# Performance work log

Measured on AMD Instinct MI355X. Metric: run time of the kernel, lower is better.

Reference implementation:

```python
import jax, jax.numpy as jnp
import numpy as np
import math

B, S, D, H = 4, 2048, 1024, 16
HD = D // H  # head_dim = 64


def _rope_tables(max_len, half_dim, theta=10000.0):
    inv_freq = 1.0 / (theta ** (jnp.arange(0, half_dim, dtype=jnp.float32) / half_dim))
    ang = jnp.arange(max_len, dtype=jnp.float32)[:, None] * inv_freq[None, :]  # [max_len, half_dim]
    return jnp.cos(ang), jnp.sin(ang)


def _apply_rope(x, cos, sin):
    # x: [B, H, S, HD]; cos/sin: [S, HD/2]
    x1, x2 = x[..., ::2], x[..., 1::2]
    # matches torch.cat([x1*cos - x2*sin, x1*sin + x2*cos], dim=-1)
    return jnp.concatenate([x1 * cos - x2 * sin, x1 * sin + x2 * cos], axis=-1)


def setup_inputs() -> dict:
    key = jax.random.key(0)
    kx, kq, ko = jax.random.split(key, 3)
    x = jax.random.normal(kx, (B, S, D), dtype=jnp.float32)
    Wqkv = jax.random.normal(kq, (D, 3 * D), dtype=jnp.float32) / math.sqrt(D)
    Wout = jax.random.normal(ko, (D, D), dtype=jnp.float32) / math.sqrt(D)
    cos, sin = _rope_tables(S, HD // 2)
    # causal additive mask, per-batch as in module signature [B, S, S]
    causal = jnp.where(jnp.tril(jnp.ones((S, S), dtype=bool)), 0.0, -1e9).astype(jnp.float32)
    mask = jnp.broadcast_to(causal, (B, S, S))
    return {"x": x, "cos": cos, "sin": sin, "mask": mask, "Wqkv": Wqkv, "Wout": Wout}


def reference(x, cos, sin, mask, Wqkv, Wout):
    b, s, d = x.shape
    qkv = x @ Wqkv  # [B, S, 3D]
    q, k, v = jnp.split(qkv, 3, axis=-1)
    def to_heads(t):
        return t.reshape(b, s, H, HD).transpose(0, 2, 1, 3)  # [B, H, S, HD]
    q, k, v = to_heads(q), to_heads(k), to_heads(v)
    q = _apply_rope(q, cos[:s], sin[:s])
    k = _apply_rope(k, cos[:s], sin[:s])
    scores = jnp.einsum("bhqd,bhkd->bhqk", q, k) / math.sqrt(HD)
    attn = jax.nn.softmax(scores + mask[:, None, :, :], axis=-1)
    out = jnp.einsum("bhqk,bhkd->bhqd", attn, v)  # [B, H, S, HD]
    out = out.transpose(0, 2, 1, 3).reshape(b, s, d)
    return out @ Wout
```

## Files before the change

### kernel.cpp

```cpp
#include <hip/hip_runtime.h>
#include <hip/hip_bf16.h>
#include <stdint.h>

#define B_   4
#define S_   2048
#define D_   1024
#define H_   16
#define HD_  64
#define BH_  (B_*H_)
#define MROWS (B_*S_)

typedef short  short8  __attribute__((ext_vector_type(8)));
typedef float  floatx4 __attribute__((ext_vector_type(4)));

__device__ __forceinline__ ushort f2bf(float f) {
    union { float f; uint32_t u; } v; v.f = f;
    uint32_t u = v.u;
    return (ushort)((u + 0x7FFFu + ((u >> 16) & 1u)) >> 16);
}
__device__ __forceinline__ float u2f(uint32_t u) {
    union { uint32_t u; float f; } v; v.u = u; return v.f;
}
__device__ __forceinline__ uint32_t f2u(float f) {
    union { float f; uint32_t u; } v; v.f = f; return v.u;
}

__device__ __forceinline__ void gl_lds16(const ushort* g, ushort* l) {
    __builtin_amdgcn_global_load_lds(
        (const __attribute__((address_space(1))) unsigned int*)g,
        (__attribute__((address_space(3))) unsigned int*)l,
        16, 0, 0);
}

__global__ void k_f32_to_bf16(const float* __restrict__ in, ushort* __restrict__ out, int n) {
    int i = (blockIdx.x * blockDim.x + threadIdx.x) * 4;
    if (i + 3 < n) {
        float4 f = *(const float4*)(in + i);
        ushort4 o; o.x = f2bf(f.x); o.y = f2bf(f.y); o.z = f2bf(f.z); o.w = f2bf(f.w);
        *(ushort4*)(out + i) = o;
    }
}

__global__ void k_transpose_to_bf16(const float* __restrict__ in, ushort* __restrict__ out,
                                    int R, int C) {
    __shared__ float tile[32][33];
    int bx = blockIdx.x * 32;
    int by = blockIdx.y * 32;
    int tx = threadIdx.x;
    int ty = threadIdx.y;
    #pragma unroll
    for (int j = 0; j < 32; j += 8)
        tile[ty + j][tx] = in[(size_t)(by + ty + j) * C + bx + tx];
    __syncthreads();
    #pragma unroll
    for (int j = 0; j < 32; j += 8)
        out[(size_t)(bx + ty + j) * R + by + tx] = f2bf(tile[tx][ty + j]);
}

__global__ void k_vtrans(const ushort* __restrict__ Vb, ushort* __restrict__ VbT) {
    __shared__ __align__(16) ushort t[64 * 72];
    int bh = blockIdx.x >> 5;
    int s0 = (blockIdx.x & 31) * 64;
    int tid = threadIdx.x;
    int ss = tid >> 2, c0 = (tid & 3) * 16;
    size_t base = (size_t)bh * S_ * HD_;
    *(uint4*)&t[ss * 72 + c0]     = *(const uint4*)&Vb[base + (size_t)(s0 + ss) * HD_ + c0];
    *(uint4*)&t[ss * 72 + c0 + 8] = *(const uint4*)&Vb[base + (size_t)(s0 + ss) * HD_ + c0 + 8];
    __syncthreads();
    int hd = tid >> 2, q0 = (tid & 3) * 16;
    ushort tmp[16];
    #pragma unroll
    for (int e = 0; e < 16; e++) tmp[e] = t[(q0 + e) * 72 + hd];
    size_t obase = (size_t)bh * HD_ * S_ + (size_t)hd * S_ + s0 + q0;
    *(uint4*)&VbT[obase]     = *(const uint4*)&tmp[0];
    *(uint4*)&VbT[obase + 8] = *(const uint4*)&tmp[8];
}

#define BM 128
#define BN 128
#define BK 32
#define LDT 32

template<int EPI>
__global__ __launch_bounds__(256)
void k_gemm(const ushort* __restrict__ A, const ushort* __restrict__ Bt,
            float* __restrict__ outF,
            ushort* __restrict__ q_out, ushort* __restrict__ k_out, ushort* __restrict__ v_out,
            int M, int N, int K) {
    __shared__ __align__(16) ushort As[BM * LDT];
    __shared__ __align__(16) ushort Bs[BN * LDT];
    int tid  = threadIdx.x;
    int lane = tid & 63;
    int wave = tid >> 6;
    int quad = lane >> 4;
    int l16  = lane & 15;
    int bm = blockIdx.y * BM;
    int bn = blockIdx.x * BN;
    int wm = (wave >> 1) * 64;
    int wn = (wave & 1) * 64;

    floatx4 acc[4][4] = {};

    for (int k0 = 0; k0 < K; k0 += BK) {
        __syncthreads();
        #pragma unroll
        for (int p = 0; p < 2; p++) {
            int c   = p * 256 + tid;
            int row = c >> 2;
            int kc  = (c & 3) << 3;
            gl_lds16(&A[(size_t)(bm + row) * K + k0 + kc],  &As[c * 8]);
            gl_lds16(&Bt[(size_t)(bn + row) * K + k0 + kc], &Bs[c * 8]);
        }
        __syncthreads();
        short8 af[4], bf[4];
        #pragma unroll
        for (int mt = 0; mt < 4; mt++)
            af[mt] = *(const short8*)&As[(wm + mt * 16 + l16) * LDT + quad * 8];
        #pragma unroll
        for (int nt = 0; nt < 4; nt++)
            bf[nt] = *(const short8*)&Bs[(wn + nt * 16 + l16) * LDT + quad * 8];
        #pragma unroll
        for (int mt = 0; mt < 4; mt++)
            #pragma unroll
            for (int nt = 0; nt < 4; nt++)
                acc[mt][nt] = __builtin_amdgcn_mfma_f32_16x16x32_bf16(af[mt], bf[nt], acc[mt][nt], 0, 0, 0);
    }

    #pragma unroll
    for (int mt = 0; mt < 4; mt++)
        #pragma unroll
        for (int nt = 0; nt < 4; nt++)
            #pragma unroll
            for (int r = 0; r < 4; r++) {
                int row = bm + wm + mt * 16 + quad * 4 + r;
                int col = bn + wn + nt * 16 + l16;
                float v = acc[mt][nt][r];
                if (EPI == 0) {
                    int which = col >> 10;
                    int rem   = col & 1023;
                    int h  = rem >> 6, hd = rem & 63;
                    int b  = row >> 11, s  = row & 2047;
                    size_t idx = ((size_t)(b * H_ + h) * S_ + s) * HD_ + hd;
                    ushort bv = f2bf(v);
                    ushort* dst = (which == 0) ? q_out : (which == 1) ? k_out : v_out;
                    dst[idx] = bv;
                } else {
                    outF[(size_t)row * N + col] = v;
                }
            }
}

__global__ void k_rope(ushort* __restrict__ Q, ushort* __restrict__ Kv,
                       const float* __restrict__ cosT, const float* __restrict__ sinT) {
    int wid  = (blockIdx.x * 256 + threadIdx.x) >> 6;
    int lane = threadIdx.x & 63;
    int s  = wid & (S_ - 1);
    int bh = wid >> 11;
    int i  = lane & 31;
    float c  = cosT[s * 32 + i];
    float sn = sinT[s * 32 + i];
    size_t base = ((size_t)bh * S_ + s) * HD_;

    uint32_t uq = *(const uint32_t*)&Q[base + 2 * i];
    float x1 = u2f(uq << 16), x2 = u2f(uq & 0xFFFF0000u);
    float o  = (lane < 32) ? (x1 * c - x2 * sn) : (x1 * sn + x2 * c);
    Q[base + lane] = f2bf(o * 0.1803368801f);

    uint32_t uk = *(const uint32_t*)&Kv[base + 2 * i];
    x1 = u2f(uk << 16); x2 = u2f(uk & 0xFFFF0000u);
    o  = (lane < 32) ? (x1 * c - x2 * sn) : (x1 * sn + x2 * c);
    Kv[base + lane] = f2bf(o);
}

__global__ __launch_bounds__(256, 4)
void k_attn(const ushort* __restrict__ Q, const ushort* __restrict__ K,
            const ushort* __restrict__ VT, ushort* __restrict__ O) {
    __shared__ __align__(16) ushort Ksp[2][64 * 32];
    __shared__ __align__(16) ushort Vtp[2][64 * 32];
    __shared__ __align__(16) ushort Pst[4][32 * 72];

    int tid  = threadIdx.x;
    int lane = tid & 63;
    int wave = tid >> 6;
    int quad = lane >> 4;
    int l16  = lane & 15;

    int bh   = blockIdx.x & 63;
    int qblk = 15 - (blockIdx.x >> 6);
    int qb0  = qblk * 128;
    size_t hbase = (size_t)bh * S_ * HD_;
    size_t vbase = (size_t)bh * HD_ * S_;

    int mrow[2] = { qb0 + wave * 16, qb0 + 64 + wave * 16 };

    short8 qf[2][2];
    #pragma unroll
    for (int m = 0; m < 2; m++)
        #pragma unroll
        for (int h = 0; h < 2; h++)
            qf[m][h] = *(const short8*)&Q[hbase + (size_t)(mrow[m] + l16) * HD_ + quad * 8 + h * 32];

    short8 ones;
    #pragma unroll
    for (int e = 0; e < 8; e++) ones[e] = (short)0x3F80;

    floatx4 acc[2][4] = {};
    floatx4 accl[2] = {};

    int crow = tid >> 2;
    int coff = (tid & 3) * 8;

    int nk = 2 * qblk + 2;
    for (int kb = 0; kb < nk; kb++) {
        int k0 = kb * 64;
        __syncthreads();
        #pragma unroll
        for (int h = 0; h < 2; h++)
            gl_lds16(&K[hbase + (size_t)(k0 + crow) * HD_ + h * 32 + coff], &Ksp[h][tid * 8]);
        #pragma unroll
        for (int k2 = 0; k2 < 2; k2++)
            gl_lds16(&VT[vbase + (size_t)crow * S_ + k0 + k2 * 32 + coff], &Vtp[k2][tid * 8]);
        __syncthreads();

        bool act[2] = { k0 <= mrow[0] + 15, k0 <= mrow[1] + 15 };

        #pragma unroll
        for (int m = 0; m < 2; m++) {
            if (!act[m]) continue;
            floatx4 sc[4] = {};
            #pragma unroll
            for (int kt = 0; kt < 4; kt++)
                #pragma unroll
                for (int h = 0; h < 2; h++) {
                    short8 kf = *(const short8*)&Ksp[h][(kt * 16 + l16) * 32 + quad * 8];
                    sc[kt] = __builtin_amdgcn_mfma_f32_16x16x32_bf16(kf, qf[m][h], sc[kt], 0, 0, 0);
                }
            bool needMask = (k0 + 63 > mrow[m]);
            int qr = mrow[m] + l16;
            #pragma unroll
            for (int kt = 0; kt < 4; kt++) {
                float p[4];
                #pragma unroll
                for (int r = 0; r < 4; r++) {
                    float v = exp2f(sc[kt][r]);
                    if (needMask) {
                        int kc = k0 + kt * 16 + quad * 4 + r;
                        if (kc > qr) v = 0.0f;
                    }
                    p[r] = v;
                }
                uint2 pk;
                pk.x = __builtin_amdgcn_perm(f2u(p[1]) + 0x8000u, f2u(p[0]) + 0x8000u, 0x07060302u);
                pk.y = __builtin_amdgcn_perm(f2u(p[3]) + 0x8000u, f2u(p[2]) + 0x8000u, 0x07060302u);
                *(uint2*)&Pst[wave][(m * 16 + l16) * 72 + kt * 16 + quad * 4] = pk;
            }
        }

        #pragma unroll
        for (int k2 = 0; k2 < 2; k2++) {
            #pragma unroll
            for (int m = 0; m < 2; m++) {
                if (!act[m]) continue;
                short8 pa = *(const short8*)&Pst[wave][(m * 16 + l16) * 72 + k2 * 32 + quad * 8];
                #pragma unroll
                for (int nt = 0; nt < 4; nt++) {
                    short8 vb = *(const short8*)&Vtp[k2][(nt * 16 + l16) * 32 + quad * 8];
                    acc[m][nt] = __builtin_amdgcn_mfma_f32_16x16x32_bf16(pa, vb, acc[m][nt], 0, 0, 0);
                }
                accl[m] = __builtin_amdgcn_mfma_f32_16x16x32_bf16(pa, ones, accl[m], 0, 0, 0);
            }
        }
    }

    int b = bh >> 4, h = bh & 15;
    #pragma unroll
    for (int m = 0; m < 2; m++)
        #pragma unroll
        for (int r = 0; r < 4; r++) {
            float inv = 1.0f / accl[m][r];
            int qr = mrow[m] + quad * 4 + r;
            #pragma unroll
            for (int nt = 0; nt < 4; nt++)
                O[((size_t)(b * S_ + qr)) * D_ + h * HD_ + nt * 16 + l16] = f2bf(acc[m][nt][r] * inv);
        }
}

extern "C" void kernel_launch(void* const* d_in, const int* in_sizes, int n_in,
                              void* d_out, int out_size, void* d_ws, size_t ws_size,
                              hipStream_t stream) {
    const float* x    = (const float*)d_in[0];
    const float* cosT = (const float*)d_in[1];
    const float* sinT = (const float*)d_in[2];
    const float* Wqkv = (const float*)d_in[4];
    const float* Wout = (const float*)d_in[5];
    float* out = (float*)d_out;

    ushort* ws = (ushort*)d_ws;
    ushort* Xbf    = ws;
    ushort* WqkvT  = Xbf    + (size_t)MROWS * D_;
    ushort* WoutT  = WqkvT  + (size_t)3 * D_ * D_;
    ushort* Qb     = WoutT  + (size_t)D_ * D_;
    ushort* Kb     = Qb     + (size_t)BH_ * S_ * HD_;
    ushort* Vb     = Kb     + (size_t)BH_ * S_ * HD_;
    ushort* VbT    = Vb     + (size_t)BH_ * S_ * HD_;
    ushort* AO     = Xbf;

    k_f32_to_bf16<<<(MROWS * D_) / 1024, 256, 0, stream>>>(x, Xbf, MROWS * D_);
    k_transpose_to_bf16<<<dim3(3 * D_ / 32, D_ / 32), dim3(32, 8), 0, stream>>>(Wqkv, WqkvT, D_, 3 * D_);
    k_transpose_to_bf16<<<dim3(D_ / 32, D_ / 32), dim3(32, 8), 0, stream>>>(Wout, WoutT, D_, D_);
    k_gemm<0><<<dim3(3 * D_ / BN, MROWS / BM), 256, 0, stream>>>(Xbf, WqkvT, nullptr, Qb, Kb, Vb,
                                                                 MROWS, 3 * D_, D_);
    k_rope<<<(BH_ * S_ * 64) / 256, 256, 0, stream>>>(Qb, Kb, cosT, sinT);
    k_vtrans<<<BH_ * 32, 256, 0, stream>>>(Vb, VbT);
    k_attn<<<1024, 256, 0, stream>>>(Qb, Kb, VbT, AO);
    k_gemm<1><<<dim3(D_ / BN, MROWS / BM), 256, 0, stream>>>(AO, WoutT, out, nullptr, nullptr, nullptr,
                                                             MROWS, D_, D_);
}
```

Before: 333.7 us.

## Use XOR-swizzled LDS layouts with BK=64 in GEMM and attention

The GEMM K-tile grows from 32 to 64 and A/B tiles are stored in LDS with an XOR swizzle on 16-byte chunks, which halves the number of K-loop iterations and barriers. The attention kernel's K and V^T tiles become single 64x64 swizzled arrays, and the P staging buffer switches from padded rows to an XOR-swizzled layout. V fragments are hoisted out of the m loop so they are loaded once and reused for both row blocks. The aim is to cut LDS bank conflicts and sync overhead, at the cost of more LDS per block and more address arithmetic.

```diff
diff --git a/kernel.cpp b/kernel.cpp
--- a/kernel.cpp
+++ b/kernel.cpp
@@ -78,8 +78,7 @@
 
 #define BM 128
 #define BN 128
-#define BK 32
-#define LDT 32
+#define BK 64
 
 template<int EPI>
 __global__ __launch_bounds__(256)
@@ -87,8 +86,8 @@
             float* __restrict__ outF,
             ushort* __restrict__ q_out, ushort* __restrict__ k_out, ushort* __restrict__ v_out,
             int M, int N, int K) {
-    __shared__ __align__(16) ushort As[BM * LDT];
-    __shared__ __align__(16) ushort Bs[BN * LDT];
+    __shared__ __align__(16) ushort As[BM * 64];
+    __shared__ __align__(16) ushort Bs[BN * 64];
     int tid  = threadIdx.x;
     int lane = tid & 63;
     int wave = tid >> 6;
@@ -104,26 +103,31 @@
     for (int k0 = 0; k0 < K; k0 += BK) {
         __syncthreads();
         #pragma unroll
-        for (int p = 0; p < 2; p++) {
-            int c   = p * 256 + tid;
-            int row = c >> 2;
-            int kc  = (c & 3) << 3;
-            gl_lds16(&A[(size_t)(bm + row) * K + k0 + kc],  &As[c * 8]);
-            gl_lds16(&Bt[(size_t)(bn + row) * K + k0 + kc], &Bs[c * 8]);
+        for (int i = 0; i < 4; i++) {
+            int c   = i * 256 + tid;
+            int row = c >> 3;
+            int gc  = (c & 7) ^ (row & 7);
+            gl_lds16(&A[(size_t)(bm + row) * K + k0 + gc * 8],  &As[c * 8]);
+            gl_lds16(&Bt[(size_t)(bn + row) * K + k0 + gc * 8], &Bs[c * 8]);
         }
         __syncthreads();
-        short8 af[4], bf[4];
-        #pragma unroll
-        for (int mt = 0; mt < 4; mt++)
-            af[mt] = *(const short8*)&As[(wm + mt * 16 + l16) * LDT + quad * 8];
-        #pragma unroll
-        for (int nt = 0; nt < 4; nt++)
-            bf[nt] = *(const short8*)&Bs[(wn + nt * 16 + l16) * LDT + quad * 8];
-        #pragma unroll
-        for (int mt = 0; mt < 4; mt++)
+        #pragma unroll
+        for (int kk = 0; kk < 2; kk++) {
+            short8 af[4], bf[4];
+            #pragma unroll
+            for (int mt = 0; mt < 4; mt++)
+                af[mt] = *(const short8*)&As[(wm + mt * 16 + l16) * 64 +
+                                             (((kk * 4 + quad) ^ (l16 & 7)) << 3)];
             #pragma unroll
             for (int nt = 0; nt < 4; nt++)
-                acc[mt][nt] = __builtin_amdgcn_mfma_f32_16x16x32_bf16(af[mt], bf[nt], acc[mt][nt], 0, 0, 0);
+                bf[nt] = *(const short8*)&Bs[(wn + nt * 16 + l16) * 64 +
+                                             (((kk * 4 + quad) ^ (l16 & 7)) << 3)];
+            #pragma unroll
+            for (int mt = 0; mt < 4; mt++)
+                #pragma unroll
+                for (int nt = 0; nt < 4; nt++)
+                    acc[mt][nt] = __builtin_amdgcn_mfma_f32_16x16x32_bf16(af[mt], bf[nt], acc[mt][nt], 0, 0, 0);
+        }
     }
 
     #pragma unroll
@@ -175,9 +179,9 @@
 __global__ __launch_bounds__(256, 4)
 void k_attn(const ushort* __restrict__ Q, const ushort* __restrict__ K,
             const ushort* __restrict__ VT, ushort* __restrict__ O) {
-    __shared__ __align__(16) ushort Ksp[2][64 * 32];
-    __shared__ __align__(16) ushort Vtp[2][64 * 32];
-    __shared__ __align__(16) ushort Pst[4][32 * 72];
+    __shared__ __align__(16) ushort Ks[64 * 64];
+    __shared__ __align__(16) ushort Vt[64 * 64];
+    __shared__ __align__(16) ushort Pst[4][32 * 64];
 
     int tid  = threadIdx.x;
     int lane = tid & 63;
@@ -207,19 +211,18 @@
     floatx4 acc[2][4] = {};
     floatx4 accl[2] = {};
 
-    int crow = tid >> 2;
-    int coff = (tid & 3) * 8;
-
     int nk = 2 * qblk + 2;
     for (int kb = 0; kb < nk; kb++) {
         int k0 = kb * 64;
         __syncthreads();
         #pragma unroll
-        for (int h = 0; h < 2; h++)
-            gl_lds16(&K[hbase + (size_t)(k0 + crow) * HD_ + h * 32 + coff], &Ksp[h][tid * 8]);
-        #pragma unroll
-        for (int k2 = 0; k2 < 2; k2++)
-            gl_lds16(&VT[vbase + (size_t)crow * S_ + k0 + k2 * 32 + coff], &Vtp[k2][tid * 8]);
+        for (int i = 0; i < 2; i++) {
+            int c   = i * 256 + tid;
+            int row = c >> 3;
+            int gc  = (c & 7) ^ (row & 7);
+            gl_lds16(&K[hbase + (size_t)(k0 + row) * HD_ + gc * 8], &Ks[c * 8]);
+            gl_lds16(&VT[vbase + (size_t)row * S_ + k0 + gc * 8],   &Vt[c * 8]);
+        }
         __syncthreads();
 
         bool act[2] = { k0 <= mrow[0] + 15, k0 <= mrow[1] + 15 };
@@ -232,7 +235,8 @@
             for (int kt = 0; kt < 4; kt++)
                 #pragma unroll
                 for (int h = 0; h < 2; h++) {
-                    short8 kf = *(const short8*)&Ksp[h][(kt * 16 + l16) * 32 + quad * 8];
+                    short8 kf = *(const short8*)&Ks[(kt * 16 + l16) * 64 +
+                                                    (((h * 4 + quad) ^ (l16 & 7)) << 3)];
                     sc[kt] = __builtin_amdgcn_mfma_f32_16x16x32_bf16(kf, qf[m][h], sc[kt], 0, 0, 0);
                 }
             bool needMask = (k0 + 63 > mrow[m]);
@@ -252,21 +256,26 @@
                 uint2 pk;
                 pk.x = __builtin_amdgcn_perm(f2u(p[1]) + 0x8000u, f2u(p[0]) + 0x8000u, 0x07060302u);
                 pk.y = __builtin_amdgcn_perm(f2u(p[3]) + 0x8000u, f2u(p[2]) + 0x8000u, 0x07060302u);
-                *(uint2*)&Pst[wave][(m * 16 + l16) * 72 + kt * 16 + quad * 4] = pk;
+                int pc = (kt * 4 + quad) ^ (l16 & 14);
+                *(uint2*)&Pst[wave][(m * 16 + l16) * 64 + pc * 4] = pk;
             }
         }
 
         #pragma unroll
         for (int k2 = 0; k2 < 2; k2++) {
+            short8 vb[4];
+            #pragma unroll
+            for (int nt = 0; nt < 4; nt++)
+                vb[nt] = *(const short8*)&Vt[(nt * 16 + l16) * 64 +
+                                             (((k2 * 4 + quad) ^ (l16 & 7)) << 3)];
             #pragma unroll
             for (int m = 0; m < 2; m++) {
                 if (!act[m]) continue;
-                short8 pa = *(const short8*)&Pst[wave][(m * 16 + l16) * 72 + k2 * 32 + quad * 8];
+                int pe = (k2 * 8 + quad * 2) ^ (l16 & 14);
+                short8 pa = *(const short8*)&Pst[wave][(m * 16 + l16) * 64 + pe * 4];
                 #pragma unroll
-                for (int nt = 0; nt < 4; nt++) {
-                    short8 vb = *(const short8*)&Vtp[k2][(nt * 16 + l16) * 32 + quad * 8];
-                    acc[m][nt] = __builtin_amdgcn_mfma_f32_16x16x32_bf16(pa, vb, acc[m][nt], 0, 0, 0);
-                }
+                for (int nt = 0; nt < 4; nt++)
+                    acc[m][nt] = __builtin_amdgcn_mfma_f32_16x16x32_bf16(pa, vb[nt], acc[m][nt], 0, 0, 0);
                 accl[m] = __builtin_amdgcn_mfma_f32_16x16x32_bf16(pa, ones, accl[m], 0, 0, 0);
             }
         }
```

Measured after the change: 311.3 us. 6.7% less time.
